# Kernel optimization log

Hardware: AMD Instinct MI355X
Metric: run time of the kernel (lower is better)

## Reference

```python
import jax, jax.numpy as jnp
import numpy as np

B, Q, E, NH, L, P = 8, 1024, 256, 8, 4, 4
DH = E // NH
SHAPES = np.array([[128, 128], [64, 64], [32, 32], [16, 16]], dtype=np.int64)
STARTS = np.concatenate([[0], np.cumsum(SHAPES.prod(1))[:-1]]).astype(np.int64)
S_TOTAL = int(SHAPES.prod(1).sum())
EPS = 1e-5


def setup_inputs() -> dict:
    key = jax.random.key(0)
    ks = iter(jax.random.split(key, 40))
    def rn(shp, s=0.02):
        return jax.random.normal(next(ks), shp, jnp.float32) * s
    return {
        "tgt": rn((B, Q, E), 1.0),
        "query_pos": rn((B, Q, E), 1.0),
        "reference_points": jax.random.uniform(next(ks), (B, Q, L, 2), jnp.float32),
        "src": rn((B, S_TOTAL, E), 1.0),
        "spatial_shapes": jnp.asarray(SHAPES),
        "level_start_index": jnp.asarray(STARTS),
        "in_proj_w": rn((3 * E, E)), "in_proj_b": jnp.zeros((3 * E,), jnp.float32),
        "out_proj_w": rn((E, E)), "out_proj_b": jnp.zeros((E,), jnp.float32),
        "norm1_g": jnp.ones((E,), jnp.float32), "norm1_b": jnp.zeros((E,), jnp.float32),
        "off_w": rn((NH * L * P * 2, E)), "off_b": rn((NH * L * P * 2,), 0.5),
        "aw_w": rn((NH * L * P, E)), "aw_b": jnp.zeros((NH * L * P,), jnp.float32),
        "vp_w": rn((E, E)), "vp_b": jnp.zeros((E,), jnp.float32),
        "op_w": rn((E, E)), "op_b": jnp.zeros((E,), jnp.float32),
        "norm2_g": jnp.ones((E,), jnp.float32), "norm2_b": jnp.zeros((E,), jnp.float32),
        "w1": rn((4 * E, E)), "b1": jnp.zeros((4 * E,), jnp.float32),
        "w2": rn((E, 4 * E)), "b2": jnp.zeros((E,), jnp.float32),
        "norm3_g": jnp.ones((E,), jnp.float32), "norm3_b": jnp.zeros((E,), jnp.float32),
    }


def _ln(x, g, b):
    mu = x.mean(-1, keepdims=True)
    var = ((x - mu) ** 2).mean(-1, keepdims=True)
    return (x - mu) * jax.lax.rsqrt(var + EPS) * g + b


def _bilinear(v, loc, Hl, Wl):
    # v: [B,NH,S_l,DH], loc in [0,1]: [B,NH,Q,P,2] -> [B,NH,Q,P,DH]
    # matches torch grid_sample(align_corners=False, padding='zeros')
    x = loc[..., 0] * Wl - 0.5
    y = loc[..., 1] * Hl - 0.5
    x0 = jnp.floor(x)
    y0 = jnp.floor(y)
    wx = (x - x0)[..., None]
    wy = (y - y0)[..., None]
    def g(yi, xi):
        valid = ((xi >= 0) & (xi <= Wl - 1) & (yi >= 0) & (yi <= Hl - 1)).astype(v.dtype)
        idx = (jnp.clip(yi, 0, Hl - 1) * Wl + jnp.clip(xi, 0, Wl - 1)).astype(jnp.int32)
        out = jnp.take_along_axis(v, idx.reshape(B, NH, Q * P, 1), axis=2)
        return out.reshape(B, NH, Q, P, DH) * valid[..., None]
    v00 = g(y0, x0); v01 = g(y0, x0 + 1.0)
    v10 = g(y0 + 1.0, x0); v11 = g(y0 + 1.0, x0 + 1.0)
    return (v00 * (1 - wy) * (1 - wx) + v01 * (1 - wy) * wx
            + v10 * wy * (1 - wx) + v11 * wy * wx)


def _forward(tgt, query_pos, reference_points, src,
             in_proj_w, in_proj_b, out_proj_w, out_proj_b, norm1_g, norm1_b,
             off_w, off_b, aw_w, aw_b, vp_w, vp_b, op_w, op_b,
             norm2_g, norm2_b, w1, b1, w2, b2, norm3_g, norm3_b,
             spatial_shapes, level_start_index):
    shp = np.asarray(spatial_shapes)
    starts = np.asarray(level_start_index)
    # ---- self-attention (q = k = tgt + pos, v = tgt) ----
    qk = tgt + query_pos
    wq, wk, wv = jnp.split(in_proj_w, 3, axis=0)
    bq, bk, bv = jnp.split(in_proj_b, 3, axis=0)
    q = (qk @ wq.T + bq).reshape(B, Q, NH, DH)
    k = (qk @ wk.T + bk).reshape(B, Q, NH, DH)
    v = (tgt @ wv.T + bv).reshape(B, Q, NH, DH)
    scores = jnp.einsum("bqhd,bkhd->bhqk", q, k) / jnp.sqrt(jnp.float32(DH))
    attn = jax.nn.softmax(scores, axis=-1)
    ctx = jnp.einsum("bhqk,bkhd->bqhd", attn, v).reshape(B, Q, E)
    tgt = _ln(tgt + (ctx @ out_proj_w.T + out_proj_b), norm1_g, norm1_b)
    # ---- MSDA cross-attention ----
    query = tgt + query_pos
    value = (src @ vp_w.T + vp_b).reshape(B, S_TOTAL, NH, DH).transpose(0, 2, 1, 3)  # [B,NH,S,DH]
    off = (query @ off_w.T + off_b).reshape(B, Q, NH, L, P, 2)
    aw = jax.nn.softmax((query @ aw_w.T + aw_b).reshape(B, Q, NH, L * P), -1)
    aw = aw.reshape(B, Q, NH, L, P)
    normalizer = jnp.asarray(shp[:, ::-1].copy(), jnp.float32)  # [L,2] = (W,H)
    loc = reference_points[:, :, None, :, None, :] + off / normalizer[None, None, None, :, None, :]
    loc = jnp.transpose(loc, (0, 2, 1, 3, 4, 5))  # [B,NH,Q,L,P,2]
    awt = jnp.transpose(aw, (0, 2, 1, 3, 4))      # [B,NH,Q,L,P]
    out = jnp.zeros((B, NH, Q, DH), jnp.float32)
    for l in range(L):
        Hl, Wl = int(shp[l, 0]), int(shp[l, 1])
        s0 = int(starts[l])
        vl = value[:, :, s0:s0 + Hl * Wl]
        samp = _bilinear(vl, loc[:, :, :, l], Hl, Wl)         # [B,NH,Q,P,DH]
        out = out + (samp * awt[:, :, :, l, :, None]).sum(3)
    ca = out.transpose(0, 2, 1, 3).reshape(B, Q, E) @ op_w.T + op_b
    tgt = _ln(tgt + ca, norm2_g, norm2_b)
    # ---- FFN ----
    h = jax.nn.relu(tgt @ w1.T + b1) @ w2.T + b2
    return _ln(tgt + h, norm3_g, norm3_b)


def reference(tgt, query_pos, reference_points, src, spatial_shapes, level_start_index,
              in_proj_w, in_proj_b, out_proj_w, out_proj_b, norm1_g, norm1_b,
              off_w, off_b, aw_w, aw_b, vp_w, vp_b, op_w, op_b,
              norm2_g, norm2_b, w1, b1, w2, b2, norm3_g, norm3_b):
    return _forward(tgt, query_pos, reference_points, src,
                    in_proj_w, in_proj_b, out_proj_w, out_proj_b, norm1_g, norm1_b,
                    off_w, off_b, aw_w, aw_b, vp_w, vp_b, op_w, op_b,
                    norm2_g, norm2_b, w1, b1, w2, b2, norm3_g, norm3_b,
                    spatial_shapes, level_start_index)
```

## Files before the change

### kernel.cpp

```cpp
#include <hip/hip_runtime.h>
#include <hip/hip_bf16.h>
#include <math.h>

typedef __hip_bfloat16 bf16;
typedef unsigned short ushort_t;

#define BQ 8
#define QLEN 1024
#define EMB 256
#define NHD 8
#define NLVL 4
#define NPT 4
#define DHD 32
#define STOT 21760

typedef short s8v __attribute__((ext_vector_type(8)));
typedef float f4v __attribute__((ext_vector_type(4)));

__device__ __forceinline__ float b2f(bf16 x) { return __bfloat162float(x); }

__device__ __forceinline__ float ldin(const void* p, int bf, size_t i) {
    return bf ? __bfloat162float(((const bf16*)p)[i]) : ((const float*)p)[i];
}

__device__ __forceinline__ float bfraw(unsigned u) {
    union { unsigned i; float f; } c; c.i = u << 16; return c.f;
}

__device__ __forceinline__ unsigned short f2us(float x) {
    bf16 h = __float2bfloat16(x);
    unsigned short u;
    __builtin_memcpy(&u, &h, 2);
    return u;
}

typedef const __attribute__((address_space(1))) unsigned int* gas1_u32;
typedef __attribute__((address_space(3))) unsigned int* las3_u32;
__device__ __forceinline__ void gload_lds16(const void* g, void* l) {
    __builtin_amdgcn_global_load_lds((gas1_u32)g, (las3_u32)l, 16, 0, 0);
}

__global__ void detect_dtype(const unsigned* __restrict__ n1g, int* __restrict__ flag) {
    if (threadIdx.x == 0) flag[0] = (n1g[0] == 0x3F800000u) ? 0 : 1;
}

template <bool ARAW, bool RELU, typename CT, int WR, int WC>
__global__ __launch_bounds__(64 * WR * WC) void gemm_mfma(
        const void* __restrict__ A,
        const void* __restrict__ W, int w0,
        const void* __restrict__ bias, int b0,
        CT* __restrict__ C,
        int M, int N, int K,
        const int* __restrict__ dflag) {
    constexpr int T = 64 * WR * WC;
    constexpr int NW = WR * WC;
    constexpr int BM = 64 * WR, BN = 64 * WC;
    constexpr int ACH = (BM * 4) / T;
    constexpr int BCH = (BN * 4) / T;
    constexpr int STAGE_US = (BM + BN) * 32;
    constexpr int EPI_US = NW * 16 * 88;
    constexpr int SMEM_US = STAGE_US > EPI_US ? STAGE_US : EPI_US;

    const int bfm = *dflag;
    __shared__ __align__(16) ushort_t smem[SMEM_US];
    ushort_t* As = smem;
    ushort_t* Bs = smem + BM * 32;

    const int tid = threadIdx.x;
    const int lane = tid & 63;
    const int wv = tid >> 6;
    const int wrow = (wv % WR) << 6;
    const int wcol = (wv / WR) << 6;
    const int m0 = blockIdx.x * BM, n0 = blockIdx.y * BN;
    const int l15 = lane & 15, lhi = lane >> 4;
    const int swz = (l15 >> 1) & 3;

    f4v acc[4][4] = {};

    auto stage = [&](int k0) {
#pragma unroll
        for (int i = 0; i < ACH; ++i) {
            const int s0 = (wv << 6) + T * i;
            const int s = s0 + lane;
            const int r = s >> 2;
            const int gd = (s & 3) ^ ((r >> 1) & 3);
            const size_t aoff = (size_t)(m0 + r) * K + k0 + gd * 8;
            if (!ARAW || bfm) {
                gload_lds16((const ushort_t*)A + aoff, As + (size_t)s0 * 8);
            } else {
                const float* af = (const float*)A + aoff;
                const float4 f0 = *(const float4*)af;
                const float4 f1 = *(const float4*)(af + 4);
                ushort_t t[8] = {f2us(f0.x), f2us(f0.y), f2us(f0.z), f2us(f0.w),
                                 f2us(f1.x), f2us(f1.y), f2us(f1.z), f2us(f1.w)};
                *(uint4*)(As + (size_t)s * 8) = *(uint4*)t;
            }
        }
#pragma unroll
        for (int i = 0; i < BCH; ++i) {
            const int s0 = (wv << 6) + T * i;
            const int s = s0 + lane;
            const int r = s >> 2;
            const int gd = (s & 3) ^ ((r >> 1) & 3);
            const size_t woff = (size_t)(w0 + n0 + r) * K + k0 + gd * 8;
            if (bfm) {
                gload_lds16((const ushort_t*)W + woff, Bs + (size_t)s0 * 8);
            } else {
                const float* wf = (const float*)W + woff;
                const float4 f0 = *(const float4*)wf;
                const float4 f1 = *(const float4*)(wf + 4);
                ushort_t t[8] = {f2us(f0.x), f2us(f0.y), f2us(f0.z), f2us(f0.w),
                                 f2us(f1.x), f2us(f1.y), f2us(f1.z), f2us(f1.w)};
                *(uint4*)(Bs + (size_t)s * 8) = *(uint4*)t;
            }
        }
    };

    for (int k0 = 0; k0 < K; k0 += 32) {
        stage(k0);
        __syncthreads();

        s8v afr[4], bfr[4];
#pragma unroll
        for (int i = 0; i < 4; ++i)
            afr[i] = *(const s8v*)(As + (wrow + i * 16 + l15) * 32 + ((lhi ^ swz) << 3));
#pragma unroll
        for (int j = 0; j < 4; ++j)
            bfr[j] = *(const s8v*)(Bs + (wcol + j * 16 + l15) * 32 + ((lhi ^ swz) << 3));
#pragma unroll
        for (int i = 0; i < 4; ++i)
#pragma unroll
            for (int j = 0; j < 4; ++j)
                acc[i][j] = __builtin_amdgcn_mfma_f32_16x16x32_bf16(
                    afr[i], bfr[j], acc[i][j], 0, 0, 0);
        __syncthreads();
    }

    if (sizeof(CT) == 2) {
        ushort_t* eb = smem + wv * 16 * 88;
#pragma unroll
        for (int i = 0; i < 4; ++i) {
#pragma unroll
            for (int j = 0; j < 4; ++j) {
                const int n = n0 + wcol + j * 16 + l15;
                const float bv = ldin(bias, bfm, b0 + n);
#pragma unroll
                for (int p = 0; p < 4; ++p) {
                    float v = acc[i][j][p] + bv;
                    if (RELU) v = fmaxf(v, 0.f);
                    eb[(lhi * 4 + p) * 88 + j * 16 + l15] = f2us(v);
                }
            }
#pragma unroll
            for (int pass = 0; pass < 2; ++pass) {
                const int row = pass * 8 + (lane >> 3);
                const int g = lane & 7;
                const uint4 u = *(const uint4*)(eb + row * 88 + g * 8);
                const int m = m0 + wrow + i * 16 + row;
                const int n = n0 + wcol + g * 8;
                *(uint4*)((ushort_t*)C + (size_t)m * N + n) = u;
            }
        }
    } else {
        float* ef = (float*)smem + wv * 16 * 44;
#pragma unroll
        for (int i = 0; i < 4; ++i) {
#pragma unroll
            for (int jp = 0; jp < 2; ++jp) {
#pragma unroll
                for (int j2 = 0; j2 < 2; ++j2) {
                    const int j = jp * 2 + j2;
                    const int n = n0 + wcol + j * 16 + l15;
                    const float bv = ldin(bias, bfm, b0 + n);
#pragma unroll
                    for (int p = 0; p < 4; ++p) {
                        float v = acc[i][j][p] + bv;
                        if (RELU) v = fmaxf(v, 0.f);
                        ef[(lhi * 4 + p) * 44 + j2 * 16 + l15] = v;
                    }
                }
#pragma unroll
                for (int pass = 0; pass < 2; ++pass) {
                    const int row = pass * 8 + (lane >> 3);
                    const int g = lane & 7;
                    const float4 u = *(const float4*)(ef + row * 44 + g * 4);
                    const int m = m0 + wrow + i * 16 + row;
                    const int n = n0 + wcol + jp * 32 + g * 4;
                    *(float4*)((float*)C + (size_t)m * N + n) = u;
                }
            }
        }
    }
}

__global__ void ew_add_bf(const void* __restrict__ a, const void* __restrict__ b,
                          ushort_t* __restrict__ c, int n, const int* __restrict__ dflag) {
    const int bfm = *dflag;
    int i = blockIdx.x * 256 + threadIdx.x;
    if (i < n) c[i] = f2us(ldin(a, bfm, i) + ldin(b, bfm, i));
}

__global__ __launch_bounds__(256) void attn_mfma(const ushort_t* __restrict__ qkbuf,
                                                 const ushort_t* __restrict__ v,
                                                 ushort_t* __restrict__ ctx) {
    __shared__ ushort_t Ks[64][40];
    __shared__ ushort_t Vt[32][72];
    __shared__ ushort_t Ps[4][16][72];
    const int bh = blockIdx.y;
    const int b = bh >> 3, h = bh & 7;
    const int qt = blockIdx.x;
    const int tid = threadIdx.x;
    const int lane = tid & 63;
    const int wv = tid >> 6;
    const int l15 = lane & 15, quad = lane >> 4;
    const float scale = 0.17677669529663689f;

    const int qbase = (qt << 6) + (wv << 4);
    const s8v qfrag = *(const s8v*)(qkbuf +
        ((size_t)(b * QLEN + qbase + l15)) * 512 + h * DHD + quad * 8);

    const int sk = tid >> 2;
    const int sd = (tid & 3) << 3;

    float m_run[4] = {-1e30f, -1e30f, -1e30f, -1e30f};
    float l_run[4] = {};
    f4v o[2] = {};

    for (int kt = 0; kt < 16; ++kt) {
        __syncthreads();
        const size_t krow = (size_t)(b * QLEN + (kt << 6) + sk);
        *(uint4*)&Ks[sk][sd] = *(const uint4*)(qkbuf + krow * 512 + 256 + h * DHD + sd);
        const uint4 uv = *(const uint4*)(v + krow * 256 + h * DHD + sd);
        ushort_t vt[8];
        *(uint4*)vt = uv;
#pragma unroll
        for (int j = 0; j < 8; ++j) Vt[sd + j][sk] = vt[j];
        __syncthreads();

        f4v s4[4];
#pragma unroll
        for (int kb = 0; kb < 4; ++kb) {
            const s8v kfr = *(const s8v*)&Ks[(kb << 4) + l15][quad * 8];
            s4[kb] = __builtin_amdgcn_mfma_f32_16x16x32_bf16(qfrag, kfr, f4v{}, 0, 0, 0);
        }

        float sc[4][4];
#pragma unroll
        for (int kb = 0; kb < 4; ++kb)
#pragma unroll
            for (int p = 0; p < 4; ++p) sc[kb][p] = s4[kb][p] * scale;
        float mp[4];
#pragma unroll
        for (int p = 0; p < 4; ++p)
            mp[p] = fmaxf(fmaxf(sc[0][p], sc[1][p]), fmaxf(sc[2][p], sc[3][p]));
#pragma unroll
        for (int p = 0; p < 4; ++p) {
            mp[p] = fmaxf(mp[p], __shfl_xor(mp[p], 1, 64));
            mp[p] = fmaxf(mp[p], __shfl_xor(mp[p], 2, 64));
            mp[p] = fmaxf(mp[p], __shfl_xor(mp[p], 4, 64));
            mp[p] = fmaxf(mp[p], __shfl_xor(mp[p], 8, 64));
        }
        float al[4], ls[4] = {};
#pragma unroll
        for (int p = 0; p < 4; ++p) {
            const float mn = fmaxf(m_run[p], mp[p]);
            al[p] = __expf(m_run[p] - mn);
            m_run[p] = mn;
        }
        float pe[4][4];
#pragma unroll
        for (int kb = 0; kb < 4; ++kb)
#pragma unroll
            for (int p = 0; p < 4; ++p) {
                const float e = __expf(sc[kb][p] - m_run[p]);
                pe[kb][p] = e;
                ls[p] += e;
            }
#pragma unroll
        for (int p = 0; p < 4; ++p) {
            ls[p] += __shfl_xor(ls[p], 1, 64);
            ls[p] += __shfl_xor(ls[p], 2, 64);
            ls[p] += __shfl_xor(ls[p], 4, 64);
            ls[p] += __shfl_xor(ls[p], 8, 64);
            l_run[p] = l_run[p] * al[p] + ls[p];
        }
#pragma unroll
        for (int nb = 0; nb < 2; ++nb)
#pragma unroll
            for (int p = 0; p < 4; ++p) o[nb][p] *= al[p];

#pragma unroll
        for (int kb = 0; kb < 4; ++kb)
#pragma unroll
            for (int p = 0; p < 4; ++p)
                Ps[wv][(quad << 2) + p][(kb << 4) + l15] = f2us(pe[kb][p]);

#pragma unroll
        for (int kk = 0; kk < 2; ++kk) {
            const s8v afr = *(const s8v*)&Ps[wv][l15][kk * 32 + quad * 8];
#pragma unroll
            for (int nb = 0; nb < 2; ++nb) {
                const s8v bfr = *(const s8v*)&Vt[nb * 16 + l15][kk * 32 + quad * 8];
                o[nb] = __builtin_amdgcn_mfma_f32_16x16x32_bf16(afr, bfr, o[nb], 0, 0, 0);
            }
        }
    }

#pragma unroll
    for (int p = 0; p < 4; ++p) {
        const float inv = 1.f / l_run[p];
        const size_t row = (size_t)(b * QLEN + qbase + (quad << 2) + p) * EMB + h * DHD;
#pragma unroll
        for (int nb = 0; nb < 2; ++nb)
            ctx[row + nb * 16 + l15] = f2us(o[nb][p] * inv);
    }
}

__global__ __launch_bounds__(256) void ln_kernel(const void* __restrict__ xb,
                                                 const float* __restrict__ xf1,
                                                 const float* __restrict__ xf2,
                                                 const void* __restrict__ g,
                                                 const void* __restrict__ bta,
                                                 float* __restrict__ out_f,
                                                 ushort_t* __restrict__ out_b,
                                                 void* __restrict__ out_d,
                                                 const void* __restrict__ qp,
                                                 ushort_t* __restrict__ out_q,
                                                 const int* __restrict__ dflag) {
    const int bf = *dflag;
    const int row = blockIdx.x, t = threadIdx.x;
    const size_t base = (size_t)row * EMB + t;
    float x = 0.f;
    if (xb) x += ldin(xb, bf, base);
    if (xf1) x += xf1[base];
    if (xf2) x += xf2[base];
    __shared__ float red[256];
    red[t] = x;
    __syncthreads();
    for (int o = 128; o > 0; o >>= 1) { if (t < o) red[t] += red[t + o]; __syncthreads(); }
    const float mu = red[0] * (1.f / EMB);
    __syncthreads();
    const float dx = x - mu;
    red[t] = dx * dx;
    __syncthreads();
    for (int o = 128; o > 0; o >>= 1) { if (t < o) red[t] += red[t + o]; __syncthreads(); }
    const float var = red[0] * (1.f / EMB);
    const float y = dx * rsqrtf(var + 1e-5f) * ldin(g, bf, t) + ldin(bta, bf, t);
    if (out_f) out_f[base] = y;
    if (out_b) out_b[base] = f2us(y);
    if (out_d) {
        if (bf) ((ushort_t*)out_d)[base] = f2us(y);
        else    ((float*)out_d)[base] = y;
    }
    if (out_q) out_q[base] = f2us(y + ldin(qp, bf, base));
}

__global__ __launch_bounds__(64) void sample_kernel(const float* __restrict__ offb,
                                                    const float* __restrict__ awb,
                                                    const void* __restrict__ refp,
                                                    const ushort_t* __restrict__ value,
                                                    ushort_t* __restrict__ out,
                                                    const int* __restrict__ dflag) {
    const int bf = *dflag;
    const int bid = blockIdx.x;
    const int h = bid & 7;
    const int bq = bid >> 3;
    const int b = bq >> 10;
    const int lane = threadIdx.x;
    const int s_idx = lane >> 2;
    const int dg = lane & 3;
    const int l = s_idx >> 2;

    float logit = awb[(size_t)bq * 128 + h * 16 + s_idx];
    float m = logit;
#pragma unroll
    for (int o = 32; o > 0; o >>= 1) m = fmaxf(m, __shfl_xor(m, o, 64));
    float e = __expf(logit - m);
    float ssum = e;
#pragma unroll
    for (int o = 32; o > 0; o >>= 1) ssum += __shfl_xor(ssum, o, 64);
    const float paw = 4.f * e / ssum;

    const int Wi = 128 >> l;
    const float Wl = (float)Wi, Hl = (float)Wi;
    const int s0 = (l == 0) ? 0 : (l == 1) ? 16384 : (l == 2) ? 20480 : 21504;

    const float rx = ldin(refp, bf, ((size_t)bq * NLVL + l) * 2 + 0);
    const float ry = ldin(refp, bf, ((size_t)bq * NLVL + l) * 2 + 1);
    const float ox = offb[(size_t)bq * 256 + h * 32 + s_idx * 2 + 0];
    const float oy = offb[(size_t)bq * 256 + h * 32 + s_idx * 2 + 1];
    const float x = (rx + ox / Wl) * Wl - 0.5f;
    const float y = (ry + oy / Hl) * Hl - 0.5f;
    const float x0 = floorf(x), y0 = floorf(y);
    const float wx = x - x0, wy = y - y0;

    float acc[8] = {};
    const ushort_t* vbase = value + ((size_t)b * STOT) * EMB + h * DHD + dg * 8;

    auto corner = [&](float yi, float xi, float w) {
        const bool valid = (xi >= 0.f) && (xi <= Wl - 1.f) && (yi >= 0.f) && (yi <= Hl - 1.f);
        const float xc = fminf(fmaxf(xi, 0.f), Wl - 1.f);
        const float yc = fminf(fmaxf(yi, 0.f), Hl - 1.f);
        const int row = s0 + (int)yc * Wi + (int)xc;
        const uint4 u = *(const uint4*)(vbase + (size_t)row * EMB);
        const float wv = valid ? w : 0.f;
        const unsigned ua[4] = {u.x, u.y, u.z, u.w};
#pragma unroll
        for (int j = 0; j < 4; ++j) {
            acc[2 * j + 0] = fmaf(wv, bfraw(ua[j] & 0xffffu), acc[2 * j + 0]);
            acc[2 * j + 1] = fmaf(wv, bfraw(ua[j] >> 16), acc[2 * j + 1]);
        }
    };
    corner(y0, x0, (1.f - wy) * (1.f - wx));
    corner(y0, x0 + 1.f, (1.f - wy) * wx);
    corner(y0 + 1.f, x0, wy * (1.f - wx));
    corner(y0 + 1.f, x0 + 1.f, wy * wx);

#pragma unroll
    for (int j = 0; j < 8; ++j) {
        float vj = acc[j] * paw;
        vj += __shfl_xor(vj, 4, 64);
        vj += __shfl_xor(vj, 8, 64);
        vj += __shfl_xor(vj, 16, 64);
        vj += __shfl_xor(vj, 32, 64);
        acc[j] = vj;
    }
    if (s_idx == 0) {
        ushort_t t[8];
#pragma unroll
        for (int j = 0; j < 8; ++j) t[j] = f2us(acc[j]);
        *(uint4*)(out + (size_t)bq * EMB + h * DHD + dg * 8) = *(uint4*)t;
    }
}

extern "C" void kernel_launch(void* const* d_in, const int* in_sizes, int n_in,
                              void* d_out, int out_size, void* d_ws, size_t ws_size,
                              hipStream_t stream) {
    const void* tgt  = d_in[0];
    const void* qp   = d_in[1];
    const void* refp = d_in[2];
    const void* src  = d_in[3];
    const void* ipw  = d_in[6];
    const void* ipb  = d_in[7];
    const void* oprw = d_in[8];
    const void* oprb = d_in[9];
    const void* n1g  = d_in[10];
    const void* n1b  = d_in[11];
    const void* ofw  = d_in[12];
    const void* ofb  = d_in[13];
    const void* aww  = d_in[14];
    const void* awbv = d_in[15];
    const void* vpw  = d_in[16];
    const void* vpb  = d_in[17];
    const void* opw2 = d_in[18];
    const void* opb2 = d_in[19];
    const void* n2g  = d_in[20];
    const void* n2b  = d_in[21];
    const void* w1   = d_in[22];
    const void* b1   = d_in[23];
    const void* w2   = d_in[24];
    const void* b2   = d_in[25];
    const void* n3g  = d_in[26];
    const void* n3b  = d_in[27];

    const int M = BQ * QLEN;
    const int MS = BQ * STOT;

    char* ws = (char*)d_ws;
    int* dflag = (int*)ws;
    size_t o = 256;
    char* S1 = ws + o; o += (size_t)M * EMB * 2;
    char* S2 = ws + o; o += (size_t)M * 512 * 2;
    char* S3 = ws + o; o += (size_t)M * EMB * 2;
    char* S4 = ws + o; o += (size_t)M * EMB * 2;
    char* S5 = ws + o; o += (size_t)M * EMB * 4;
    char* S6 = ws + o; o += (size_t)M * EMB * 4;
    char* S7 = ws + o; o += (size_t)M * EMB * 4;
    char* S8 = ws + o;

    ushort_t* qk_bf    = (ushort_t*)S1;
    ushort_t* samp_bf  = (ushort_t*)S1;
    ushort_t* qkproj   = (ushort_t*)S2;
    float*    off_f    = (float*)S2;
    ushort_t* vproj    = (ushort_t*)S3;
    ushort_t* qry_bf   = (ushort_t*)S3;
    ushort_t* tgt2_bf  = (ushort_t*)S3;
    ushort_t* ctx_bf   = (ushort_t*)S4;
    float*    awl_f    = (float*)S4;
    float*    bufD     = (float*)S5;
    float*    tgt1_f   = (float*)S6;
    float*    tgt2_f   = (float*)S7;
    ushort_t* value_bf = (ushort_t*)S8;
    ushort_t* h1_bf    = (ushort_t*)S8;

    detect_dtype<<<1, 64, 0, stream>>>((const unsigned*)n1g, dflag);

    ew_add_bf<<<(M * EMB) / 256, 256, 0, stream>>>(tgt, qp, qk_bf, M * EMB, dflag);
    gemm_mfma<false, false, ushort_t, 1, 2><<<dim3(M / 64, 4), 128, 0, stream>>>(
        qk_bf, ipw, 0, ipb, 0, qkproj, M, 512, 256, dflag);
    gemm_mfma<true, false, ushort_t, 1, 2><<<dim3(M / 64, 2), 128, 0, stream>>>(
        tgt, ipw, 512, ipb, 512, vproj, M, 256, 256, dflag);
    attn_mfma<<<dim3(16, BQ * NHD), 256, 0, stream>>>(qkproj, vproj, ctx_bf);
    gemm_mfma<false, false, float, 1, 2><<<dim3(M / 64, 2), 128, 0, stream>>>(
        ctx_bf, oprw, 0, oprb, 0, bufD, M, 256, 256, dflag);
    ln_kernel<<<M, 256, 0, stream>>>(tgt, bufD, nullptr, n1g, n1b,
                                     tgt1_f, nullptr, nullptr, qp, qry_bf, dflag);

    gemm_mfma<false, false, float, 1, 2><<<dim3(M / 64, 2), 128, 0, stream>>>(
        qry_bf, ofw, 0, ofb, 0, off_f, M, 256, 256, dflag);
    gemm_mfma<false, false, float, 1, 2><<<dim3(M / 64, 1), 128, 0, stream>>>(
        qry_bf, aww, 0, awbv, 0, awl_f, M, 128, 256, dflag);
    gemm_mfma<true, false, ushort_t, 2, 4><<<dim3(MS / 128, 1), 512, 0, stream>>>(
        src, vpw, 0, vpb, 0, value_bf, MS, 256, 256, dflag);
    sample_kernel<<<M * NHD, 64, 0, stream>>>(off_f, awl_f, refp, value_bf, samp_bf, dflag);
    gemm_mfma<false, false, float, 1, 2><<<dim3(M / 64, 2), 128, 0, stream>>>(
        samp_bf, opw2, 0, opb2, 0, bufD, M, 256, 256, dflag);
    ln_kernel<<<M, 256, 0, stream>>>(nullptr, tgt1_f, bufD, n2g, n2b,
                                     tgt2_f, tgt2_bf, nullptr, nullptr, nullptr, dflag);

    gemm_mfma<false, true, ushort_t, 1, 2><<<dim3(M / 64, 8), 128, 0, stream>>>(
        tgt2_bf, w1, 0, b1, 0, h1_bf, M, 1024, 256, dflag);
    gemm_mfma<false, false, float, 1, 2><<<dim3(M / 64, 2), 128, 0, stream>>>(
        h1_bf, w2, 0, b2, 0, bufD, M, 256, 1024, dflag);
    ln_kernel<<<M, 256, 0, stream>>>(nullptr, tgt2_f, bufD, n3g, n3b,
                                     nullptr, nullptr, d_out, nullptr, nullptr, dflag);
}
```

Measured before the change: 738.3 us.

## Use single-wave double-buffered GEMM tiles and vectorize layernorm and add kernels

Replaces the multi-wave GEMM with a single-wave 64x64 tile kernel. It double-buffers the LDS tiles with direct global-to-LDS loads, waits on counters instead of block barriers, and swaps the grid order so N is the fast axis. The elementwise add and layernorm kernels now process four elements per thread. Layernorm runs one row per wave with shuffle reductions in place of shared-memory tree reductions. Smaller tiles give more blocks and overlap loads with MFMA work, at the cost of less tile reuse per block and relying on manual vmcnt counting, which only holds when the data is bf16.

```diff
diff --git a/kernel.cpp b/kernel.cpp
--- a/kernel.cpp
+++ b/kernel.cpp
@@ -34,6 +34,17 @@
     return u;
 }
 
+__device__ __forceinline__ void ld4(const void* p, int bf, size_t i, float* o) {
+    if (bf) {
+        const uint2 u = *(const uint2*)((const ushort_t*)p + i);
+        o[0] = bfraw(u.x & 0xffffu); o[1] = bfraw(u.x >> 16);
+        o[2] = bfraw(u.y & 0xffffu); o[3] = bfraw(u.y >> 16);
+    } else {
+        const float4 f = *(const float4*)((const float*)p + i);
+        o[0] = f.x; o[1] = f.y; o[2] = f.z; o[3] = f.w;
+    }
+}
+
 typedef const __attribute__((address_space(1))) unsigned int* gas1_u32;
 typedef __attribute__((address_space(3))) unsigned int* las3_u32;
 __device__ __forceinline__ void gload_lds16(const void* g, void* l) {
@@ -44,105 +55,104 @@
     if (threadIdx.x == 0) flag[0] = (n1g[0] == 0x3F800000u) ? 0 : 1;
 }
 
-template <bool ARAW, bool RELU, typename CT, int WR, int WC>
-__global__ __launch_bounds__(64 * WR * WC) void gemm_mfma(
+template <bool ARAW, bool RELU, typename CT>
+__global__ __launch_bounds__(64) void gemm64(
         const void* __restrict__ A,
         const void* __restrict__ W, int w0,
         const void* __restrict__ bias, int b0,
         CT* __restrict__ C,
         int M, int N, int K,
         const int* __restrict__ dflag) {
-    constexpr int T = 64 * WR * WC;
-    constexpr int NW = WR * WC;
-    constexpr int BM = 64 * WR, BN = 64 * WC;
-    constexpr int ACH = (BM * 4) / T;
-    constexpr int BCH = (BN * 4) / T;
-    constexpr int STAGE_US = (BM + BN) * 32;
-    constexpr int EPI_US = NW * 16 * 88;
-    constexpr int SMEM_US = STAGE_US > EPI_US ? STAGE_US : EPI_US;
-
     const int bfm = *dflag;
-    __shared__ __align__(16) ushort_t smem[SMEM_US];
-    ushort_t* As = smem;
-    ushort_t* Bs = smem + BM * 32;
-
-    const int tid = threadIdx.x;
-    const int lane = tid & 63;
-    const int wv = tid >> 6;
-    const int wrow = (wv % WR) << 6;
-    const int wcol = (wv / WR) << 6;
-    const int m0 = blockIdx.x * BM, n0 = blockIdx.y * BN;
+    __shared__ __align__(16) ushort_t smem[2][2 * 64 * 32];
+
+    const int lane = threadIdx.x;
+    const int n0 = blockIdx.x * 64, m0 = blockIdx.y * 64;
     const int l15 = lane & 15, lhi = lane >> 4;
     const int swz = (l15 >> 1) & 3;
+    const int nt = K >> 5;
 
     f4v acc[4][4] = {};
 
-    auto stage = [&](int k0) {
-#pragma unroll
-        for (int i = 0; i < ACH; ++i) {
-            const int s0 = (wv << 6) + T * i;
-            const int s = s0 + lane;
+    auto stage = [&](int t, int buf) {
+        const int k0 = t << 5;
+        ushort_t* As = smem[buf];
+        ushort_t* Bs = smem[buf] + 64 * 32;
+#pragma unroll
+        for (int i = 0; i < 4; ++i) {
+            const int s = (i << 6) + lane;
             const int r = s >> 2;
             const int gd = (s & 3) ^ ((r >> 1) & 3);
             const size_t aoff = (size_t)(m0 + r) * K + k0 + gd * 8;
             if (!ARAW || bfm) {
-                gload_lds16((const ushort_t*)A + aoff, As + (size_t)s0 * 8);
+                gload_lds16((const ushort_t*)A + aoff, As + (size_t)(i << 6) * 8);
             } else {
                 const float* af = (const float*)A + aoff;
                 const float4 f0 = *(const float4*)af;
                 const float4 f1 = *(const float4*)(af + 4);
-                ushort_t t[8] = {f2us(f0.x), f2us(f0.y), f2us(f0.z), f2us(f0.w),
-                                 f2us(f1.x), f2us(f1.y), f2us(f1.z), f2us(f1.w)};
-                *(uint4*)(As + (size_t)s * 8) = *(uint4*)t;
-            }
-        }
-#pragma unroll
-        for (int i = 0; i < BCH; ++i) {
-            const int s0 = (wv << 6) + T * i;
-            const int s = s0 + lane;
+                ushort_t tt[8] = {f2us(f0.x), f2us(f0.y), f2us(f0.z), f2us(f0.w),
+                                  f2us(f1.x), f2us(f1.y), f2us(f1.z), f2us(f1.w)};
+                *(uint4*)(As + (size_t)s * 8) = *(uint4*)tt;
+            }
+        }
+#pragma unroll
+        for (int i = 0; i < 4; ++i) {
+            const int s = (i << 6) + lane;
             const int r = s >> 2;
             const int gd = (s & 3) ^ ((r >> 1) & 3);
             const size_t woff = (size_t)(w0 + n0 + r) * K + k0 + gd * 8;
             if (bfm) {
-                gload_lds16((const ushort_t*)W + woff, Bs + (size_t)s0 * 8);
+                gload_lds16((const ushort_t*)W + woff, Bs + (size_t)(i << 6) * 8);
             } else {
                 const float* wf = (const float*)W + woff;
                 const float4 f0 = *(const float4*)wf;
                 const float4 f1 = *(const float4*)(wf + 4);
-                ushort_t t[8] = {f2us(f0.x), f2us(f0.y), f2us(f0.z), f2us(f0.w),
-                                 f2us(f1.x), f2us(f1.y), f2us(f1.z), f2us(f1.w)};
-                *(uint4*)(Bs + (size_t)s * 8) = *(uint4*)t;
+                ushort_t tt[8] = {f2us(f0.x), f2us(f0.y), f2us(f0.z), f2us(f0.w),
+                                  f2us(f1.x), f2us(f1.y), f2us(f1.z), f2us(f1.w)};
+                *(uint4*)(Bs + (size_t)s * 8) = *(uint4*)tt;
             }
         }
     };
 
-    for (int k0 = 0; k0 < K; k0 += 32) {
-        stage(k0);
-        __syncthreads();
-
+    stage(0, 0);
+    stage(nt > 1 ? 1 : 0, 1);
+    for (int t = 0; t < nt; ++t) {
+        asm volatile("s_waitcnt vmcnt(8)" ::: "memory");
+
+        const ushort_t* As = smem[t & 1];
+        const ushort_t* Bs = smem[t & 1] + 64 * 32;
         s8v afr[4], bfr[4];
 #pragma unroll
         for (int i = 0; i < 4; ++i)
-            afr[i] = *(const s8v*)(As + (wrow + i * 16 + l15) * 32 + ((lhi ^ swz) << 3));
+            afr[i] = *(const s8v*)(As + (i * 16 + l15) * 32 + ((lhi ^ swz) << 3));
 #pragma unroll
         for (int j = 0; j < 4; ++j)
-            bfr[j] = *(const s8v*)(Bs + (wcol + j * 16 + l15) * 32 + ((lhi ^ swz) << 3));
+            bfr[j] = *(const s8v*)(Bs + (j * 16 + l15) * 32 + ((lhi ^ swz) << 3));
+
+        asm volatile("s_waitcnt lgkmcnt(0)" ::: "memory");
+        __builtin_amdgcn_sched_barrier(0);
+
+        const int tn = t + 2 < nt ? t + 2 : nt - 1;
+        stage(tn, t & 1);
+
 #pragma unroll
         for (int i = 0; i < 4; ++i)
 #pragma unroll
             for (int j = 0; j < 4; ++j)
                 acc[i][j] = __builtin_amdgcn_mfma_f32_16x16x32_bf16(
                     afr[i], bfr[j], acc[i][j], 0, 0, 0);
-        __syncthreads();
-    }
+    }
+
+    asm volatile("s_waitcnt vmcnt(0)" ::: "memory");
+    __builtin_amdgcn_sched_barrier(0);
 
     if (sizeof(CT) == 2) {
-        ushort_t* eb = smem + wv * 16 * 88;
+        ushort_t* eb = smem[0];
 #pragma unroll
         for (int i = 0; i < 4; ++i) {
 #pragma unroll
             for (int j = 0; j < 4; ++j) {
-                const int n = n0 + wcol + j * 16 + l15;
+                const int n = n0 + j * 16 + l15;
                 const float bv = ldin(bias, bfm, b0 + n);
 #pragma unroll
                 for (int p = 0; p < 4; ++p) {
@@ -156,13 +166,14 @@
                 const int row = pass * 8 + (lane >> 3);
                 const int g = lane & 7;
                 const uint4 u = *(const uint4*)(eb + row * 88 + g * 8);
-                const int m = m0 + wrow + i * 16 + row;
-                const int n = n0 + wcol + g * 8;
+                const int m = m0 + i * 16 + row;
+                const int n = n0 + g * 8;
                 *(uint4*)((ushort_t*)C + (size_t)m * N + n) = u;
             }
+            asm volatile("s_waitcnt lgkmcnt(0)" ::: "memory");
         }
     } else {
-        float* ef = (float*)smem + wv * 16 * 44;
+        float* ef = (float*)smem[0];
 #pragma unroll
         for (int i = 0; i < 4; ++i) {
 #pragma unroll
@@ -170,7 +181,7 @@
 #pragma unroll
                 for (int j2 = 0; j2 < 2; ++j2) {
                     const int j = jp * 2 + j2;
-                    const int n = n0 + wcol + j * 16 + l15;
+                    const int n = n0 + j * 16 + l15;
                     const float bv = ldin(bias, bfm, b0 + n);
 #pragma unroll
                     for (int p = 0; p < 4; ++p) {
@@ -184,20 +195,29 @@
                     const int row = pass * 8 + (lane >> 3);
                     const int g = lane & 7;
                     const float4 u = *(const float4*)(ef + row * 44 + g * 4);
-                    const int m = m0 + wrow + i * 16 + row;
-                    const int n = n0 + wcol + jp * 32 + g * 4;
+                    const int m = m0 + i * 16 + row;
+                    const int n = n0 + jp * 32 + g * 4;
                     *(float4*)((float*)C + (size_t)m * N + n) = u;
                 }
+                asm volatile("s_waitcnt lgkmcnt(0)" ::: "memory");
             }
         }
     }
 }
 
 __global__ void ew_add_bf(const void* __restrict__ a, const void* __restrict__ b,
-                          ushort_t* __restrict__ c, int n, const int* __restrict__ dflag) {
+                          ushort_t* __restrict__ c, int n4, const int* __restrict__ dflag) {
     const int bfm = *dflag;
-    int i = blockIdx.x * 256 + threadIdx.x;
-    if (i < n) c[i] = f2us(ldin(a, bfm, i) + ldin(b, bfm, i));
+    const int i = blockIdx.x * 256 + threadIdx.x;
+    if (i < n4) {
+        float ta[4], tb[4];
+        ld4(a, bfm, (size_t)i * 4, ta);
+        ld4(b, bfm, (size_t)i * 4, tb);
+        uint2 u;
+        u.x = (unsigned)f2us(ta[0] + tb[0]) | ((unsigned)f2us(ta[1] + tb[1]) << 16);
+        u.y = (unsigned)f2us(ta[2] + tb[2]) | ((unsigned)f2us(ta[3] + tb[3]) << 16);
+        *(uint2*)(c + (size_t)i * 4) = u;
+    }
 }
 
 __global__ __launch_bounds__(256) void attn_mfma(const ushort_t* __restrict__ qkbuf,
@@ -328,31 +348,66 @@
                                                  ushort_t* __restrict__ out_q,
                                                  const int* __restrict__ dflag) {
     const int bf = *dflag;
-    const int row = blockIdx.x, t = threadIdx.x;
-    const size_t base = (size_t)row * EMB + t;
-    float x = 0.f;
-    if (xb) x += ldin(xb, bf, base);
-    if (xf1) x += xf1[base];
-    if (xf2) x += xf2[base];
-    __shared__ float red[256];
-    red[t] = x;
-    __syncthreads();
-    for (int o = 128; o > 0; o >>= 1) { if (t < o) red[t] += red[t + o]; __syncthreads(); }
-    const float mu = red[0] * (1.f / EMB);
-    __syncthreads();
-    const float dx = x - mu;
-    red[t] = dx * dx;
-    __syncthreads();
-    for (int o = 128; o > 0; o >>= 1) { if (t < o) red[t] += red[t + o]; __syncthreads(); }
-    const float var = red[0] * (1.f / EMB);
-    const float y = dx * rsqrtf(var + 1e-5f) * ldin(g, bf, t) + ldin(bta, bf, t);
-    if (out_f) out_f[base] = y;
-    if (out_b) out_b[base] = f2us(y);
+    const int row = blockIdx.x * 4 + (threadIdx.x >> 6);
+    const int lane = threadIdx.x & 63;
+    const size_t base = (size_t)row * EMB + lane * 4;
+
+    float x[4] = {0.f, 0.f, 0.f, 0.f};
+    if (xb) {
+        float t[4]; ld4(xb, bf, base, t);
+#pragma unroll
+        for (int j = 0; j < 4; ++j) x[j] += t[j];
+    }
+    if (xf1) {
+        const float4 f = *(const float4*)(xf1 + base);
+        x[0] += f.x; x[1] += f.y; x[2] += f.z; x[3] += f.w;
+    }
+    if (xf2) {
+        const float4 f = *(const float4*)(xf2 + base);
+        x[0] += f.x; x[1] += f.y; x[2] += f.z; x[3] += f.w;
+    }
+    float s = x[0] + x[1] + x[2] + x[3];
+#pragma unroll
+    for (int o = 1; o < 64; o <<= 1) s += __shfl_xor(s, o, 64);
+    const float mu = s * (1.f / EMB);
+    float dx[4], vs = 0.f;
+#pragma unroll
+    for (int j = 0; j < 4; ++j) { dx[j] = x[j] - mu; vs += dx[j] * dx[j]; }
+#pragma unroll
+    for (int o = 1; o < 64; o <<= 1) vs += __shfl_xor(vs, o, 64);
+    const float inv = rsqrtf(vs * (1.f / EMB) + 1e-5f);
+
+    float gv[4], bv[4];
+    ld4(g, bf, (size_t)lane * 4, gv);
+    ld4(bta, bf, (size_t)lane * 4, bv);
+    float y[4];
+#pragma unroll
+    for (int j = 0; j < 4; ++j) y[j] = dx[j] * inv * gv[j] + bv[j];
+
+    if (out_f) *(float4*)(out_f + base) = float4{y[0], y[1], y[2], y[3]};
+    if (out_b) {
+        uint2 u;
+        u.x = (unsigned)f2us(y[0]) | ((unsigned)f2us(y[1]) << 16);
+        u.y = (unsigned)f2us(y[2]) | ((unsigned)f2us(y[3]) << 16);
+        *(uint2*)(out_b + base) = u;
+    }
     if (out_d) {
-        if (bf) ((ushort_t*)out_d)[base] = f2us(y);
-        else    ((float*)out_d)[base] = y;
-    }
-    if (out_q) out_q[base] = f2us(y + ldin(qp, bf, base));
+        if (bf) {
+            uint2 u;
+            u.x = (unsigned)f2us(y[0]) | ((unsigned)f2us(y[1]) << 16);
+            u.y = (unsigned)f2us(y[2]) | ((unsigned)f2us(y[3]) << 16);
+            *(uint2*)((ushort_t*)out_d + base) = u;
+        } else {
+            *(float4*)((float*)out_d + base) = float4{y[0], y[1], y[2], y[3]};
+        }
+    }
+    if (out_q) {
+        float q[4]; ld4(qp, bf, base, q);
+        uint2 u;
+        u.x = (unsigned)f2us(y[0] + q[0]) | ((unsigned)f2us(y[1] + q[1]) << 16);
+        u.y = (unsigned)f2us(y[2] + q[2]) | ((unsigned)f2us(y[3] + q[3]) << 16);
+        *(uint2*)(out_q + base) = u;
+    }
 }
 
 __global__ __launch_bounds__(64) void sample_kernel(const float* __restrict__ offb,
@@ -495,33 +550,33 @@
 
     detect_dtype<<<1, 64, 0, stream>>>((const unsigned*)n1g, dflag);
 
-    ew_add_bf<<<(M * EMB) / 256, 256, 0, stream>>>(tgt, qp, qk_bf, M * EMB, dflag);
-    gemm_mfma<false, false, ushort_t, 1, 2><<<dim3(M / 64, 4), 128, 0, stream>>>(
+    ew_add_bf<<<(M * EMB / 4) / 256, 256, 0, stream>>>(tgt, qp, qk_bf, M * EMB / 4, dflag);
+    gemm64<false, false, ushort_t><<<dim3(8, M / 64), 64, 0, stream>>>(
         qk_bf, ipw, 0, ipb, 0, qkproj, M, 512, 256, dflag);
-    gemm_mfma<true, false, ushort_t, 1, 2><<<dim3(M / 64, 2), 128, 0, stream>>>(
+    gemm64<true, false, ushort_t><<<dim3(4, M / 64), 64, 0, stream>>>(
         tgt, ipw, 512, ipb, 512, vproj, M, 256, 256, dflag);
     attn_mfma<<<dim3(16, BQ * NHD), 256, 0, stream>>>(qkproj, vproj, ctx_bf);
-    gemm_mfma<false, false, float, 1, 2><<<dim3(M / 64, 2), 128, 0, stream>>>(
+    gemm64<false, false, float><<<dim3(4, M / 64), 64, 0, stream>>>(
         ctx_bf, oprw, 0, oprb, 0, bufD, M, 256, 256, dflag);
-    ln_kernel<<<M, 256, 0, stream>>>(tgt, bufD, nullptr, n1g, n1b,
-                                     tgt1_f, nullptr, nullptr, qp, qry_bf, dflag);
-
-    gemm_mfma<false, false, float, 1, 2><<<dim3(M / 64, 2), 128, 0, stream>>>(
+    ln_kernel<<<M / 4, 256, 0, stream>>>(tgt, bufD, nullptr, n1g, n1b,
+                                         tgt1_f, nullptr, nullptr, qp, qry_bf, dflag);
+
+    gemm64<false, false, float><<<dim3(4, M / 64), 64, 0, stream>>>(
         qry_bf, ofw, 0, ofb, 0, off_f, M, 256, 256, dflag);
-    gemm_mfma<false, false, float, 1, 2><<<dim3(M / 64, 1), 128, 0, stream>>>(
+    gemm64<false, false, float><<<dim3(2, M / 64), 64, 0, stream>>>(
         qry_bf, aww, 0, awbv, 0, awl_f, M, 128, 256, dflag);
-    gemm_mfma<true, false, ushort_t, 2, 4><<<dim3(MS / 128, 1), 512, 0, stream>>>(
+    gemm64<true, false, ushort_t><<<dim3(4, MS / 64), 64, 0, stream>>>(
         src, vpw, 0, vpb, 0, value_bf, MS, 256, 256, dflag);
     sample_kernel<<<M * NHD, 64, 0, stream>>>(off_f, awl_f, refp, value_bf, samp_bf, dflag);
-    gemm_mfma<false, false, float, 1, 2><<<dim3(M / 64, 2), 128, 0, stream>>>(
+    gemm64<false, false, float><<<dim3(4, M / 64), 64, 0, stream>>>(
         samp_bf, opw2, 0, opb2, 0, bufD, M, 256, 256, dflag);
-    ln_kernel<<<M, 256, 0, stream>>>(nullptr, tgt1_f, bufD, n2g, n2b,
-                                     tgt2_f, tgt2_bf, nullptr, nullptr, nullptr, dflag);
-
-    gemm_mfma<false, true, ushort_t, 1, 2><<<dim3(M / 64, 8), 128, 0, stream>>>(
+    ln_kernel<<<M / 4, 256, 0, stream>>>(nullptr, tgt1_f, bufD, n2g, n2b,
+                                         tgt2_f, tgt2_bf, nullptr, nullptr, nullptr, dflag);
+
+    gemm64<false, true, ushort_t><<<dim3(16, M / 64), 64, 0, stream>>>(
         tgt2_bf, w1, 0, b1, 0, h1_bf, M, 1024, 256, dflag);
-    gemm_mfma<false, false, float, 1, 2><<<dim3(M / 64, 2), 128, 0, stream>>>(
+    gemm64<false, false, float><<<dim3(4, M / 64), 64, 0, stream>>>(
         h1_bf, w2, 0, b2, 0, bufD, M, 256, 1024, dflag);
-    ln_kernel<<<M, 256, 0, stream>>>(nullptr, tgt2_f, bufD, n3g, n3b,
-                                     nullptr, nullptr, d_out, nullptr, nullptr, dflag);
-}
+    ln_kernel<<<M / 4, 256, 0, stream>>>(nullptr, tgt2_f, bufD, n3g, n3b,
+                                         nullptr, nullptr, d_out, nullptr, nullptr, dflag);
+}
```

After: 875.0 us. +18.5%, slower.
